# Performance work log

Measured on AMD Instinct MI355X. Metric: run time of the kernel, lower is better.

Reference implementation:

```python
import jax, jax.numpy as jnp
import numpy as np

B, N, IN, OUT, H = 8, 1024, 256, 256, 4
D = OUT // H  # head_dim = 64


def setup_inputs() -> dict:
    key = jax.random.key(0)
    k1, k2, k3, k4 = jax.random.split(key, 4)
    h = jax.random.normal(k1, (B, N, IN), dtype=jnp.float32)
    # torch Linear weight: [out, in], Wh = h @ W.T
    W = jax.random.normal(k2, (H * D, IN), dtype=jnp.float32) * (1.0 / np.sqrt(IN))
    # attention vector a: [n_heads, 2*head_dim] (xavier-uniform-ish scale)
    a = jax.random.normal(k3, (H, 2 * D), dtype=jnp.float32) * 0.1
    adj_mask = jax.random.bernoulli(k4, 0.1, (B, N, N))
    # ensure every row has at least one neighbor (self-loop) to avoid all -inf rows
    adj_mask = adj_mask | jnp.eye(N, dtype=bool)[None]
    return {"h": h, "W": W, "a": a, "adj_mask": adj_mask}


def reference(h, W, a, adj_mask):
    # Wh: [B, H, N, D]
    Wh = (h @ W.T).reshape(B, N, H, D).transpose(0, 2, 1, 3)
    # Split 'a' into src/dst halves: e_ij = leaky_relu(a_src.Wh_i + a_dst.Wh_j)
    # (mathematically identical to the original concat+einsum, without the N^2*2D tensor)
    src = jnp.einsum('bhnd,hd->bhn', Wh, a[:, :D])
    dst = jnp.einsum('bhnd,hd->bhn', Wh, a[:, D:])
    e = jax.nn.leaky_relu(src[:, :, :, None] + dst[:, :, None, :], negative_slope=0.2)
    e = jnp.where(adj_mask[:, None, :, :], e, -jnp.inf)
    att = jax.nn.softmax(e, axis=-1)
    att = jnp.where(jnp.isnan(att), 0.0, att)
    # dropout in eval mode -> identity
    h_prime = jnp.einsum('bhij,bhjd->bhid', att, Wh)
    # concat=True: [B, N, H*D]
    return h_prime.transpose(0, 2, 1, 3).reshape(B, N, H * D)
```

## Files before the change

kernel.cpp:

```cpp
#include <hip/hip_runtime.h>
#include <hip/hip_bf16.h>

#define B 8
#define N 1024
#define IN 256
#define H 4
#define D 64
#define O 256
#define BN (B*N)

typedef __attribute__((ext_vector_type(4))) float f32x4;
typedef __attribute__((ext_vector_type(8))) short short8;
typedef __attribute__((ext_vector_type(4))) short short4v;

__device__ __forceinline__ short f2bf(float f){
  __hip_bfloat16 b = __float2bfloat16(f);
  return __builtin_bit_cast(short, b);
}

#define PACK_BLOCKS 1024
#define CVT_BLOCKS  1056
#define H_ELEMS (BN*IN)
__global__ __launch_bounds__(256) void k_prep(const int* __restrict__ adj,
                                              unsigned* __restrict__ bits,
                                              const float* __restrict__ hmat,
                                              const float* __restrict__ Wmat,
                                              short* __restrict__ hbf,
                                              short* __restrict__ wbf){
  if(blockIdx.x < PACK_BLOCKS){
    int t = blockIdx.x * 256 + threadIdx.x;
    const int4* p = (const int4*)(adj + ((size_t)t << 5));
    unsigned word = 0;
    #pragma unroll
    for(int k = 0; k < 8; k++){
      int4 m = p[k];
      word |= (m.x != 0 ? 1u : 0u) << (k*4 + 0);
      word |= (m.y != 0 ? 1u : 0u) << (k*4 + 1);
      word |= (m.z != 0 ? 1u : 0u) << (k*4 + 2);
      word |= (m.w != 0 ? 1u : 0u) << (k*4 + 3);
    }
    bits[t] = word;
  } else {
    int idx = (blockIdx.x - PACK_BLOCKS) * 256 + threadIdx.x;
    int e = idx * 8;
    const float* srcp; short* dstp;
    if(e < H_ELEMS){ srcp = hmat + e; dstp = hbf + e; }
    else           { srcp = Wmat + (e - H_ELEMS); dstp = wbf + (e - H_ELEMS); }
    float4 a0 = *(const float4*)srcp;
    float4 a1 = *(const float4*)(srcp + 4);
    short8 pk;
    pk[0]=f2bf(a0.x); pk[1]=f2bf(a0.y); pk[2]=f2bf(a0.z); pk[3]=f2bf(a0.w);
    pk[4]=f2bf(a1.x); pk[5]=f2bf(a1.y); pk[6]=f2bf(a1.z); pk[7]=f2bf(a1.w);
    *(short8*)dstp = pk;
  }
}

__global__ __launch_bounds__(256) void k_wh(const short* __restrict__ hbf,
                                            const short* __restrict__ wbf,
                                            const float* __restrict__ avec,
                                            short* __restrict__ VT,
                                            float* __restrict__ src,
                                            float* __restrict__ dst){
  const int t = threadIdx.x;
  const int hh = t >> 6, lane = t & 63, quad = lane >> 4, l16 = lane & 15;
  const int mbase = blockIdx.x * 16;
  f32x4 acc[4];
  #pragma unroll
  for(int x=0;x<4;x++) acc[x] = (f32x4){0.f,0.f,0.f,0.f};
  const short* ap = hbf + (size_t)(mbase + l16) * IN + quad * 8;
  const short* bp0 = wbf + (size_t)(hh * 64 + l16) * IN + quad * 8;
  #pragma unroll
  for(int kk = 0; kk < 8; kk++){
    const int k0 = kk * 32;
    short8 A = *(const short8*)(ap + k0);
    #pragma unroll
    for(int dt=0; dt<4; dt++){
      short8 Bf = *(const short8*)(bp0 + (size_t)dt*16*IN + k0);
      acc[dt] = __builtin_amdgcn_mfma_f32_16x16x32_bf16(A, Bf, acc[dt], 0, 0, 0);
    }
  }
  const int bb = mbase >> 10;
  const int nb = (mbase & (N-1)) + quad * 4;
  const int bh = bb * H + hh;
  #pragma unroll
  for(int dt=0; dt<4; dt++){
    int d = dt*16 + l16;
    short4v pk;
    pk[0]=f2bf(acc[dt][0]); pk[1]=f2bf(acc[dt][1]);
    pk[2]=f2bf(acc[dt][2]); pk[3]=f2bf(acc[dt][3]);
    *(short4v*)(VT + (((size_t)bh * D + d) << 10) + nb) = pk;
  }
  float as[4], ad[4];
  #pragma unroll
  for(int dt=0; dt<4; dt++){
    as[dt] = avec[hh*(2*D) + dt*16 + l16];
    ad[dt] = avec[hh*(2*D) + D + dt*16 + l16];
  }
  #pragma unroll
  for(int r=0; r<4; r++){
    float s = 0.f, dd = 0.f;
    #pragma unroll
    for(int dt=0; dt<4; dt++){ s += acc[dt][r]*as[dt]; dd += acc[dt][r]*ad[dt]; }
    #pragma unroll
    for(int off=1; off<16; off<<=1){
      s  += __shfl_xor(s, off, 64);
      dd += __shfl_xor(dd, off, 64);
    }
    if(l16 == 0){
      int n = nb + r;
      src[(size_t)bh * N + n] = s;
      dst[(size_t)bh * N + n] = dd;
    }
  }
}

__global__ __launch_bounds__(256, 4) void k_attn(const short* __restrict__ VT,
                                              const float* __restrict__ src,
                                              const float* __restrict__ dst,
                                              const unsigned* __restrict__ bits,
                                              float* __restrict__ out){
  __shared__ float dsh[N];
  const int t = threadIdx.x;
  const int wave = t >> 6, lane = t & 63, quad = lane >> 4, l16 = lane & 15;
  const int b = blockIdx.z, hh = blockIdx.y;
  const int bh = b * H + hh;
  const int i0 = blockIdx.x * 64;
  #pragma unroll
  for(int j = t; j < N; j += 256) dsh[j] = dst[(size_t)bh * N + j];
  const int i = i0 + wave * 16 + l16;
  const float si = src[(size_t)bh * N + i];
  const int4* mp = (const int4*)(bits + ((size_t)b * N + i) * 32);
  int4 mv[8];
  #pragma unroll
  for(int k=0;k<8;k++) mv[k] = mp[k];
  const unsigned* mw = (const unsigned*)mv;
  const short* vrow = VT + (((size_t)bh * D) << 10) + quad * 8;
  short8 ones;
  #pragma unroll
  for(int k=0;k<8;k++) ones[k] = (short)0x3F80;
  f32x4 acc[4], accl;
  #pragma unroll
  for(int x=0;x<4;x++) acc[x] = (f32x4){0.f,0.f,0.f,0.f};
  accl = (f32x4){0.f,0.f,0.f,0.f};
  short8 buf[3][4];
  #pragma unroll
  for(int pre=0; pre<2; pre++)
    #pragma unroll
    for(int dt=0; dt<4; dt++)
      buf[pre][dt] = *(const short8*)(vrow + (((size_t)(dt*16 + l16)) << 10) + pre*32);
  __syncthreads();
  #pragma unroll
  for(int jt = 0; jt < 32; jt++){
    const int cur = jt % 3, nxt = (jt + 2) % 3;
    if(jt + 2 < 32){
      #pragma unroll
      for(int dt=0; dt<4; dt++)
        buf[nxt][dt] = *(const short8*)(vrow + (((size_t)(dt*16 + l16)) << 10) + (jt+2)*32);
    }
    const int j0 = jt * 32;
    const unsigned word = mw[jt];
    float4 d0 = *(const float4*)&dsh[j0 + quad*8];
    float4 d1 = *(const float4*)&dsh[j0 + quad*8 + 4];
    float dv[8] = {d0.x,d0.y,d0.z,d0.w,d1.x,d1.y,d1.z,d1.w};
    short8 P;
    #pragma unroll
    for(int jj=0; jj<8; jj++){
      float e = si + dv[jj];
      e = fmaxf(e, 0.2f * e);
      float p = ((word >> (quad*8 + jj)) & 1u) ? __expf(e) : 0.f;
      P[jj] = f2bf(p);
    }
    accl = __builtin_amdgcn_mfma_f32_16x16x32_bf16(P, ones, accl, 0, 0, 0);
    #pragma unroll
    for(int dt=0; dt<4; dt++)
      acc[dt] = __builtin_amdgcn_mfma_f32_16x16x32_bf16(P, buf[cur][dt], acc[dt], 0, 0, 0);
  }
  #pragma unroll
  for(int r=0; r<4; r++){
    float inv = 1.0f / accl[r];
    int ig = i0 + wave*16 + quad*4 + r;
    float* op = out + ((size_t)b * N + ig) * O + hh * D + l16;
    #pragma unroll
    for(int dt=0; dt<4; dt++) op[dt*16] = acc[dt][r] * inv;
  }
}

extern "C" void kernel_launch(void* const* d_in, const int* in_sizes, int n_in,
                              void* d_out, int out_size, void* d_ws, size_t ws_size,
                              hipStream_t stream) {
  const float* hmat = (const float*)d_in[0];
  const float* Wmat = (const float*)d_in[1];
  const float* avec = (const float*)d_in[2];
  const int* adj    = (const int*)d_in[3];
  float* out = (float*)d_out;
  char* ws = (char*)d_ws;
  short*    VT    = (short*)   (ws);
  short*    hbf   = (short*)   (ws + (size_t) 4*1024*1024);
  short*    wbf   = (short*)   (ws + (size_t) 8*1024*1024);
  unsigned* bits  = (unsigned*)(ws + (size_t) 9*1024*1024);
  float*    src   = (float*)   (ws + (size_t)10*1024*1024);
  float*    dst   = (float*)   (ws + (size_t)10*1024*1024 + 131072);
  k_prep<<<PACK_BLOCKS + CVT_BLOCKS, 256, 0, stream>>>(adj, bits, hmat, Wmat, hbf, wbf);
  k_wh<<<BN/16, 256, 0, stream>>>(hbf, wbf, avec, VT, src, dst);
  k_attn<<<dim3(16, H, B), 256, 0, stream>>>(VT, src, dst, bits, out);
}
```

Measured before the change: 130.1 us.

## Fuse bf16 conversion into projection GEMM and merge prep kernels into one launch

Removes the separate fp32-to-bf16 conversion pass for h and W. The projection GEMM now reads fp32 directly and converts in registers. The mask bit-packing and projection work are merged into one kernel launch using disjoint block ranges, which removes one launch and the round trip of the bf16 intermediate buffers. In exchange, the GEMM blocks read twice as many bytes per fragment, and W is converted redundantly in every block.

```diff
diff --git a/kernel.cpp b/kernel.cpp
--- a/kernel.cpp
+++ b/kernel.cpp
@@ -19,14 +19,14 @@
 }
 
 #define PACK_BLOCKS 1024
-#define CVT_BLOCKS  1056
-#define H_ELEMS (BN*IN)
-__global__ __launch_bounds__(256) void k_prep(const int* __restrict__ adj,
-                                              unsigned* __restrict__ bits,
-                                              const float* __restrict__ hmat,
-                                              const float* __restrict__ Wmat,
-                                              short* __restrict__ hbf,
-                                              short* __restrict__ wbf){
+__global__ __launch_bounds__(256) void k_fused(const int* __restrict__ adj,
+                                               unsigned* __restrict__ bits,
+                                               const float* __restrict__ hmat,
+                                               const float* __restrict__ Wmat,
+                                               const float* __restrict__ avec,
+                                               short* __restrict__ VT,
+                                               float* __restrict__ src,
+                                               float* __restrict__ dst){
   if(blockIdx.x < PACK_BLOCKS){
     int t = blockIdx.x * 256 + threadIdx.x;
     const int4* p = (const int4*)(adj + ((size_t)t << 5));
@@ -40,42 +40,32 @@
       word |= (m.w != 0 ? 1u : 0u) << (k*4 + 3);
     }
     bits[t] = word;
-  } else {
-    int idx = (blockIdx.x - PACK_BLOCKS) * 256 + threadIdx.x;
-    int e = idx * 8;
-    const float* srcp; short* dstp;
-    if(e < H_ELEMS){ srcp = hmat + e; dstp = hbf + e; }
-    else           { srcp = Wmat + (e - H_ELEMS); dstp = wbf + (e - H_ELEMS); }
-    float4 a0 = *(const float4*)srcp;
-    float4 a1 = *(const float4*)(srcp + 4);
-    short8 pk;
-    pk[0]=f2bf(a0.x); pk[1]=f2bf(a0.y); pk[2]=f2bf(a0.z); pk[3]=f2bf(a0.w);
-    pk[4]=f2bf(a1.x); pk[5]=f2bf(a1.y); pk[6]=f2bf(a1.z); pk[7]=f2bf(a1.w);
-    *(short8*)dstp = pk;
+    return;
   }
-}
-
-__global__ __launch_bounds__(256) void k_wh(const short* __restrict__ hbf,
-                                            const short* __restrict__ wbf,
-                                            const float* __restrict__ avec,
-                                            short* __restrict__ VT,
-                                            float* __restrict__ src,
-                                            float* __restrict__ dst){
   const int t = threadIdx.x;
   const int hh = t >> 6, lane = t & 63, quad = lane >> 4, l16 = lane & 15;
-  const int mbase = blockIdx.x * 16;
+  const int mbase = (blockIdx.x - PACK_BLOCKS) * 16;
   f32x4 acc[4];
   #pragma unroll
   for(int x=0;x<4;x++) acc[x] = (f32x4){0.f,0.f,0.f,0.f};
-  const short* ap = hbf + (size_t)(mbase + l16) * IN + quad * 8;
-  const short* bp0 = wbf + (size_t)(hh * 64 + l16) * IN + quad * 8;
+  const float* ap  = hmat + (size_t)(mbase + l16) * IN + quad * 8;
+  const float* bp0 = Wmat + (size_t)(hh * 64 + l16) * IN + quad * 8;
   #pragma unroll
   for(int kk = 0; kk < 8; kk++){
     const int k0 = kk * 32;
-    short8 A = *(const short8*)(ap + k0);
+    float4 a0 = *(const float4*)(ap + k0);
+    float4 a1 = *(const float4*)(ap + k0 + 4);
+    short8 A;
+    A[0]=f2bf(a0.x); A[1]=f2bf(a0.y); A[2]=f2bf(a0.z); A[3]=f2bf(a0.w);
+    A[4]=f2bf(a1.x); A[5]=f2bf(a1.y); A[6]=f2bf(a1.z); A[7]=f2bf(a1.w);
     #pragma unroll
     for(int dt=0; dt<4; dt++){
-      short8 Bf = *(const short8*)(bp0 + (size_t)dt*16*IN + k0);
+      const float* bp = bp0 + (size_t)dt*16*IN + k0;
+      float4 b0 = *(const float4*)bp;
+      float4 b1 = *(const float4*)(bp + 4);
+      short8 Bf;
+      Bf[0]=f2bf(b0.x); Bf[1]=f2bf(b0.y); Bf[2]=f2bf(b0.z); Bf[3]=f2bf(b0.w);
+      Bf[4]=f2bf(b1.x); Bf[5]=f2bf(b1.y); Bf[6]=f2bf(b1.z); Bf[7]=f2bf(b1.w);
       acc[dt] = __builtin_amdgcn_mfma_f32_16x16x32_bf16(A, Bf, acc[dt], 0, 0, 0);
     }
   }
@@ -195,12 +185,9 @@
   float* out = (float*)d_out;
   char* ws = (char*)d_ws;
   short*    VT    = (short*)   (ws);
-  short*    hbf   = (short*)   (ws + (size_t) 4*1024*1024);
-  short*    wbf   = (short*)   (ws + (size_t) 8*1024*1024);
   unsigned* bits  = (unsigned*)(ws + (size_t) 9*1024*1024);
   float*    src   = (float*)   (ws + (size_t)10*1024*1024);
   float*    dst   = (float*)   (ws + (size_t)10*1024*1024 + 131072);
-  k_prep<<<PACK_BLOCKS + CVT_BLOCKS, 256, 0, stream>>>(adj, bits, hmat, Wmat, hbf, wbf);
-  k_wh<<<BN/16, 256, 0, stream>>>(hbf, wbf, avec, VT, src, dst);
+  k_fused<<<PACK_BLOCKS + BN/16, 256, 0, stream>>>(adj, bits, hmat, Wmat, avec, VT, src, dst);
   k_attn<<<dim3(16, H, B), 256, 0, stream>>>(VT, src, dst, bits, out);
 }
```

Result: slower. 141.9 us (+9.1%).
